# Performance work log

Hardware: AMD Instinct MI355X
Metric: run time of the kernel (lower is better)

Reference implementation:

```python
import jax, jax.numpy as jnp
import numpy as np

DIM = 1024
N_HEADS = 16
HEAD_DIM = DIM // N_HEADS
LN_EPS = 1e-5


def layer_norm(x, gamma, beta):
    mu = jnp.mean(x, axis=-1, keepdims=True)
    var = jnp.var(x, axis=-1, keepdims=True)
    return (x - mu) * jax.lax.rsqrt(var + LN_EPS) * gamma + beta


def setup_inputs() -> dict:
    key = jax.random.key(0)
    ks = jax.random.split(key, 12)
    B, Nq, Nc, D = 2, 2048, 2048, DIM
    s = 1.0 / np.sqrt(D)
    return {
        "query": jax.random.normal(ks[0], (B, Nq, D), jnp.float32),
        "context": jax.random.normal(ks[1], (B, Nc, D), jnp.float32),
        "Wq": jax.random.normal(ks[2], (D, D), jnp.float32) * s,
        "bq": jnp.zeros((D,), jnp.float32),
        "Wk": jax.random.normal(ks[3], (D, D), jnp.float32) * s,
        "bk": jnp.zeros((D,), jnp.float32),
        "Wv": jax.random.normal(ks[4], (D, D), jnp.float32) * s,
        "bv": jnp.zeros((D,), jnp.float32),
        "Wo": jax.random.normal(ks[5], (D, D), jnp.float32) * s,
        "bo": jnp.zeros((D,), jnp.float32),
        "gq": jnp.ones((D,), jnp.float32),
        "betaq": jnp.zeros((D,), jnp.float32),
        "gkv": jnp.ones((D,), jnp.float32),
        "betakv": jnp.zeros((D,), jnp.float32),
    }


def reference(query, context, Wq, bq, Wk, bk, Wv, bv, Wo, bo, gq, betaq, gkv, betakv):
    B, Nq, D = query.shape
    Nc = context.shape[1]
    residual = query
    q = layer_norm(query, gq, betaq)
    c = layer_norm(context, gkv, betakv)
    # projections; (B,N,D) -> (B,H,N,hd)
    Q = (q @ Wq + bq).reshape(B, Nq, N_HEADS, HEAD_DIM).transpose(0, 2, 1, 3)
    K = (c @ Wk + bk).reshape(B, Nc, N_HEADS, HEAD_DIM).transpose(0, 2, 1, 3)
    V = (c @ Wv + bv).reshape(B, Nc, N_HEADS, HEAD_DIM).transpose(0, 2, 1, 3)
    scores = jnp.einsum("bhqd,bhkd->bhqk", Q, K) / np.sqrt(HEAD_DIM).astype(np.float32)
    attn = jax.nn.softmax(scores, axis=-1)
    out = jnp.einsum("bhqk,bhkd->bhqd", attn, V)
    out = out.transpose(0, 2, 1, 3).reshape(B, Nq, D)
    return residual + out @ Wo + bo
```

## Files before the change

kernel.cpp:

```cpp
#include <hip/hip_runtime.h>
#include <hip/hip_bf16.h>

typedef unsigned short u16;
typedef unsigned long long u64;
typedef __bf16 bf16x8 __attribute__((ext_vector_type(8)));
typedef float f32x4 __attribute__((ext_vector_type(4)));
typedef float f32x16 __attribute__((ext_vector_type(16)));
typedef unsigned u32x4 __attribute__((ext_vector_type(4)));

#define DIM 1024
#define NH 16
#define HD 64
#define QSCALE 0.180336880972788f

__device__ __forceinline__ u16 f2bf(float f) {
  union { float f; unsigned u; } v; v.f = f;
  unsigned r = v.u + 0x7fffu + ((v.u >> 16) & 1u);
  return (u16)(r >> 16);
}

__device__ __forceinline__ unsigned pk2(float a, float b) {
  union { __hip_bfloat162 h; unsigned u; } cv;
  cv.h = __float22bfloat162_rn(make_float2(a, b));
  return cv.u;
}

__device__ __forceinline__ float bf2f(unsigned s) {
  union { unsigned u; float f; } v; v.u = s << 16; return v.f;
}

__device__ __forceinline__ float fexp2(float x) {
#if __has_builtin(__builtin_amdgcn_exp2f)
  return __builtin_amdgcn_exp2f(x);
#else
  return exp2f(x);
#endif
}

__device__ __forceinline__ void gld16(const u16* gp, u16* lp) {
  __builtin_amdgcn_global_load_lds(
      (const __attribute__((address_space(1))) unsigned int*)(const void*)gp,
      (__attribute__((address_space(3))) unsigned int*)(void*)lp, 16, 0, 0);
}

__device__ __forceinline__ void pl32swap(unsigned& a, unsigned& b) {
  asm volatile("v_permlane32_swap_b32 %0, %1" : "+v"(a), "+v"(b));
}

__global__ __launch_bounds__(256) void prep_kernel(
    const float* __restrict__ q, const float* __restrict__ c,
    const float* __restrict__ gq, const float* __restrict__ bq,
    const float* __restrict__ gkv, const float* __restrict__ bkv,
    u16* __restrict__ qn, u16* __restrict__ cn,
    const float* W0, const float* W1, const float* W2, const float* W3,
    u16* O0, u16* O1, u16* O2, u16* O3) {
  __shared__ float red[2][4];
  __shared__ float t[32][33];
  int bid = blockIdx.x, tid = threadIdx.x;
  if (bid < 8192) {
    const float* x  = bid < 4096 ? q : c;
    const float* g  = bid < 4096 ? gq : gkv;
    const float* be = bid < 4096 ? bq : bkv;
    u16* out = bid < 4096 ? qn : cn;
    int row = bid & 4095;
    float4 v = ((const float4*)(x + (size_t)row * DIM))[tid];
    float s1 = v.x + v.y + v.z + v.w;
    float s2 = v.x * v.x + v.y * v.y + v.z * v.z + v.w * v.w;
#pragma unroll
    for (int o = 32; o >= 1; o >>= 1) { s1 += __shfl_xor(s1, o, 64); s2 += __shfl_xor(s2, o, 64); }
    int wv = tid >> 6;
    if ((tid & 63) == 0) { red[0][wv] = s1; red[1][wv] = s2; }
    __syncthreads();
    s1 = red[0][0] + red[0][1] + red[0][2] + red[0][3];
    s2 = red[1][0] + red[1][1] + red[1][2] + red[1][3];
    float mu = s1 * (1.f / DIM);
    float var = s2 * (1.f / DIM) - mu * mu;
    float rs = rsqrtf(var + 1e-5f);
    float4 gv = ((const float4*)g)[tid];
    float4 bv = ((const float4*)be)[tid];
    uint2 o2;
    o2.x = pk2((v.x - mu) * rs * gv.x + bv.x, (v.y - mu) * rs * gv.y + bv.y);
    o2.y = pk2((v.z - mu) * rs * gv.z + bv.z, (v.w - mu) * rs * gv.w + bv.w);
    ((uint2*)(out + (size_t)row * DIM))[tid] = o2;
  } else {
    int wid = bid - 8192;
    int z = wid >> 10;
    const float* W = z == 0 ? W0 : z == 1 ? W1 : z == 2 ? W2 : W3;
    u16* O        = z == 0 ? O0 : z == 1 ? O1 : z == 2 ? O2 : O3;
    int xy = wid & 1023;
    int bx = (xy & 31) * 32, by = (xy >> 5) * 32;
    int tx = tid & 31, ty = tid >> 5;
#pragma unroll
    for (int i = 0; i < 4; ++i) t[ty + i * 8][tx] = W[(size_t)(by + ty + i * 8) * DIM + bx + tx];
    __syncthreads();
#pragma unroll
    for (int i = 0; i < 4; ++i) O[(size_t)(bx + ty + i * 8) * DIM + by + tx] = f2bf(t[tx][ty + i * 8]);
  }
}

__global__ __launch_bounds__(256) void gemm_qkv(
    const u16* __restrict__ qn, const u16* __restrict__ cn,
    const u16* __restrict__ Wqt, const u16* __restrict__ Wkt, const u16* __restrict__ Wvt,
    const float* __restrict__ bq, const float* __restrict__ bk, const float* __restrict__ bv,
    u16* __restrict__ Qb, u16* __restrict__ Kb, u16* __restrict__ Vtb) {
  __shared__ __align__(16) u16 sm[(128 + 64 + 64) * 64];
  u16* As  = sm;
  u16* B0s = sm + 128 * 64;
  u16* B1s = sm + 192 * 64;
  int tid = threadIdx.x, wave = tid >> 6, lane = tid & 63;
  int lr = lane & 15, quad = lane >> 4;
  int m0 = blockIdx.x * 128, n0 = blockIdx.y * 64;
  int wm = (wave >> 1) * 64, wn = (wave & 1) * 32;

  if (blockIdx.z == 0) {
    f32x4 acck[4][2] = {}, accv[4][2] = {};
    for (int kt = 0; kt < DIM; kt += 64) {
#pragma unroll
      for (int r = 0; r < 4; ++r) {
        int slot = tid + r * 256;
        int row = slot >> 3;
        int c = (slot & 7) ^ (row & 7);
        gld16(cn + (size_t)(m0 + row) * DIM + kt + c * 8, &As[slot * 8]);
      }
      {
        int slot = tid;
        int row = slot >> 3;
        int c = (slot & 7) ^ (row & 7);
        gld16(Wkt + (size_t)(n0 + row) * DIM + kt + c * 8, &B0s[slot * 8]);
        gld16(Wvt + (size_t)(n0 + row) * DIM + kt + c * 8, &B1s[slot * 8]);
        slot = tid + 256; row = slot >> 3; c = (slot & 7) ^ (row & 7);
        gld16(Wkt + (size_t)(n0 + row) * DIM + kt + c * 8, &B0s[slot * 8]);
        gld16(Wvt + (size_t)(n0 + row) * DIM + kt + c * 8, &B1s[slot * 8]);
      }
      __syncthreads();
#pragma unroll
      for (int kc = 0; kc < 2; ++kc) {
        int pc = ((kc * 4 + quad) ^ (lr & 7)) * 8;
        bf16x8 af[4], b0f[2], b1f[2];
#pragma unroll
        for (int i = 0; i < 4; ++i) af[i] = *(const bf16x8*)&As[(wm + i * 16 + lr) * 64 + pc];
#pragma unroll
        for (int j = 0; j < 2; ++j) {
          b0f[j] = *(const bf16x8*)&B0s[(wn + j * 16 + lr) * 64 + pc];
          b1f[j] = *(const bf16x8*)&B1s[(wn + j * 16 + lr) * 64 + pc];
        }
#pragma unroll
        for (int mi = 0; mi < 4; ++mi)
#pragma unroll
          for (int ni = 0; ni < 2; ++ni) {
            acck[mi][ni] = __builtin_amdgcn_mfma_f32_16x16x32_bf16(af[mi], b0f[ni], acck[mi][ni], 0, 0, 0);
            accv[mi][ni] = __builtin_amdgcn_mfma_f32_16x16x32_bf16(b1f[ni], af[mi], accv[mi][ni], 0, 0, 0);
          }
      }
      __syncthreads();
    }
#pragma unroll
    for (int mi = 0; mi < 4; ++mi)
#pragma unroll
      for (int ni = 0; ni < 2; ++ni) {
        int col = n0 + wn + ni * 16 + lr;
        float bb_ = bk[col];
        int row0 = m0 + wm + mi * 16 + quad * 4;
#pragma unroll
        for (int r = 0; r < 4; ++r)
          Kb[(size_t)(row0 + r) * DIM + col] = f2bf(acck[mi][ni][r] + bb_);
      }
#pragma unroll
    for (int mi = 0; mi < 4; ++mi) {
      int m = m0 + wm + mi * 16 + lr;
      int bb = m >> 11, tt = m & 2047;
      u16* outb = Vtb + (((size_t)bb << 10)) * 2048 + tt;
#pragma unroll
      for (int ni = 0; ni < 2; ++ni) {
        int nbase = n0 + wn + ni * 16 + quad * 4;
#pragma unroll
        for (int r = 0; r < 4; ++r)
          outb[(size_t)(nbase + r) * 2048] = f2bf(accv[mi][ni][r] + bv[nbase + r]);
      }
    }
  } else {
    f32x4 acc[4][2] = {};
    for (int kt = 0; kt < DIM; kt += 64) {
#pragma unroll
      for (int r = 0; r < 4; ++r) {
        int slot = tid + r * 256;
        int row = slot >> 3;
        int c = (slot & 7) ^ (row & 7);
        gld16(qn + (size_t)(m0 + row) * DIM + kt + c * 8, &As[slot * 8]);
      }
#pragma unroll
      for (int r = 0; r < 2; ++r) {
        int slot = tid + r * 256;
        int row = slot >> 3;
        int c = (slot & 7) ^ (row & 7);
        gld16(Wqt + (size_t)(n0 + row) * DIM + kt + c * 8, &B0s[slot * 8]);
      }
      __syncthreads();
#pragma unroll
      for (int kc = 0; kc < 2; ++kc) {
        int pc = ((kc * 4 + quad) ^ (lr & 7)) * 8;
        bf16x8 af[4], b0f[2];
#pragma unroll
        for (int i = 0; i < 4; ++i) af[i] = *(const bf16x8*)&As[(wm + i * 16 + lr) * 64 + pc];
#pragma unroll
        for (int j = 0; j < 2; ++j) b0f[j] = *(const bf16x8*)&B0s[(wn + j * 16 + lr) * 64 + pc];
#pragma unroll
        for (int mi = 0; mi < 4; ++mi)
#pragma unroll
          for (int ni = 0; ni < 2; ++ni)
            acc[mi][ni] = __builtin_amdgcn_mfma_f32_16x16x32_bf16(af[mi], b0f[ni], acc[mi][ni], 0, 0, 0);
      }
      __syncthreads();
    }
#pragma unroll
    for (int mi = 0; mi < 4; ++mi)
#pragma unroll
      for (int ni = 0; ni < 2; ++ni) {
        int col = n0 + wn + ni * 16 + lr;
        float bb_ = bq[col];
        int row0 = m0 + wm + mi * 16 + quad * 4;
#pragma unroll
        for (int r = 0; r < 4; ++r)
          Qb[(size_t)(row0 + r) * DIM + col] = f2bf((acc[mi][ni][r] + bb_) * QSCALE);
      }
  }
}

__global__ __launch_bounds__(256) void gemm_o(const u16* __restrict__ A,
    const u16* __restrict__ Bt, const float* __restrict__ bias,
    float* __restrict__ out, const float* __restrict__ resid) {
  __shared__ __align__(16) u16 sm[(128 + 64) * 64];
  u16* As = sm;
  u16* Bs = sm + 128 * 64;
  int tid = threadIdx.x, wave = tid >> 6, lane = tid & 63;
  int lr = lane & 15, quad = lane >> 4;
  int m0 = blockIdx.x * 128, n0 = blockIdx.y * 64;
  int wm = (wave >> 1) * 64, wn = (wave & 1) * 32;
  f32x4 acc[4][2] = {};
  for (int kt = 0; kt < DIM; kt += 64) {
#pragma unroll
    for (int r = 0; r < 4; ++r) {
      int slot = tid + r * 256;
      int row = slot >> 3;
      int c = (slot & 7) ^ (row & 7);
      gld16(A + (size_t)(m0 + row) * DIM + kt + c * 8, &As[slot * 8]);
    }
#pragma unroll
    for (int r = 0; r < 2; ++r) {
      int slot = tid + r * 256;
      int row = slot >> 3;
      int c = (slot & 7) ^ (row & 7);
      gld16(Bt + (size_t)(n0 + row) * DIM + kt + c * 8, &Bs[slot * 8]);
    }
    __syncthreads();
#pragma unroll
    for (int kc = 0; kc < 2; ++kc) {
      int pc = ((kc * 4 + quad) ^ (lr & 7)) * 8;
      bf16x8 af[4], bfr[2];
#pragma unroll
      for (int i = 0; i < 4; ++i) af[i] = *(const bf16x8*)&As[(wm + i * 16 + lr) * 64 + pc];
#pragma unroll
      for (int j = 0; j < 2; ++j) bfr[j] = *(const bf16x8*)&Bs[(wn + j * 16 + lr) * 64 + pc];
#pragma unroll
      for (int mi = 0; mi < 4; ++mi)
#pragma unroll
        for (int ni = 0; ni < 2; ++ni)
          acc[mi][ni] = __builtin_amdgcn_mfma_f32_16x16x32_bf16(af[mi], bfr[ni], acc[mi][ni], 0, 0, 0);
    }
    __syncthreads();
  }
#pragma unroll
  for (int mi = 0; mi < 4; ++mi)
#pragma unroll
    for (int ni = 0; ni < 2; ++ni) {
      int col = n0 + wn + ni * 16 + lr;
      float bv = bias[col];
      int row0 = m0 + wm + mi * 16 + quad * 4;
#pragma unroll
      for (int r = 0; r < 4; ++r) {
        int row = row0 + r;
        out[(size_t)row * DIM + col] = acc[mi][ni][r] + bv + resid[(size_t)row * DIM + col];
      }
    }
}

__global__ __launch_bounds__(256, 4) void flash_kernel(const u16* __restrict__ Q,
    const u16* __restrict__ Kg, const u16* __restrict__ Vt,
    u16* __restrict__ O0, u16* __restrict__ O1,
    float* __restrict__ L0, float* __restrict__ L1) {
  __shared__ __align__(16) u16 lds[16384];
  int tid = threadIdx.x, wave = tid >> 6, lane = tid & 63;
  int ln = lane & 31, hi = lane >> 5;
  int bh = blockIdx.x, b = bh >> 4, h = bh & 15;
  int q0 = blockIdx.y * 128;
  int split = blockIdx.z;
  u16* Op = split ? O1 : O0;
  float* Lp = split ? L1 : L0;
  int t0 = split * 1024;

  const u16* kbase = Kg + (size_t)(b * 2048 + t0) * DIM + h * HD;
  const u16* vbase = Vt + (size_t)(b * 1024 + h * HD) * 2048 + t0;

  size_t qrow = (size_t)(b * 2048 + q0 + wave * 32 + ln);
  bf16x8 qf[4];
#pragma unroll
  for (int ds = 0; ds < 4; ++ds)
    qf[ds] = *(const bf16x8*)&Q[qrow * DIM + h * HD + ds * 16 + hi * 8];

  int slot0 = tid, slot1 = tid + 256;
  int r0 = slot0 >> 3, c0 = (slot0 & 7) ^ (r0 & 7);
  int r1 = slot1 >> 3, c1 = (slot1 & 7) ^ (r1 & 7);
  const u16* kp0 = kbase + (size_t)r0 * DIM + c0 * 8;
  const u16* kp1 = kbase + (size_t)r1 * DIM + c1 * 8;
  const u16* vp0 = vbase + (size_t)r0 * 2048 + c0 * 8;
  const u16* vp1 = vbase + (size_t)r1 * 2048 + c1 * 8;

  gld16(kp0, &lds[slot0 * 8]);
  gld16(kp1, &lds[slot1 * 8]);
  gld16(vp0, &lds[8192 + slot0 * 8]);
  gld16(vp1, &lds[8192 + slot1 * 8]);
  __syncthreads();

  float plsum = 0.f;
  f32x16 oacc[2] = {};

  for (int j = 0; j < 16; ++j) {
    int par = j & 1;
    const u16* kcb = &lds[par * 4096];
    const u16* vcb = &lds[8192 + par * 4096];
    if (j < 15) {
      int np = par ^ 1;
      kp0 += 64 * DIM; kp1 += 64 * DIM; vp0 += 64; vp1 += 64;
      gld16(kp0, &lds[np * 4096 + slot0 * 8]);
      gld16(kp1, &lds[np * 4096 + slot1 * 8]);
      gld16(vp0, &lds[8192 + np * 4096 + slot0 * 8]);
      gld16(vp1, &lds[8192 + np * 4096 + slot1 * 8]);
    }

    f32x16 sf[2] = {};
    __builtin_amdgcn_s_setprio(1);
#pragma unroll
    for (int kt2 = 0; kt2 < 2; ++kt2) {
      int rs = (kt2 * 32 + ln) * 64;
      int rx = (kt2 * 32 + ln) & 7;
#pragma unroll
      for (int ds = 0; ds < 4; ++ds) {
        bf16x8 kf = *(const bf16x8*)&kcb[rs + (((ds * 2 + hi) ^ rx) * 8)];
        sf[kt2] = __builtin_amdgcn_mfma_f32_32x32x16_bf16(kf, qf[ds], sf[kt2], 0, 0, 0);
      }
    }
    __builtin_amdgcn_s_setprio(0);

    bf16x8 pb[4];
#pragma unroll
    for (int kt2 = 0; kt2 < 2; ++kt2)
#pragma unroll
      for (int ks = 0; ks < 2; ++ks) {
        float e0 = fexp2(sf[kt2][ks * 8 + 0]), e1 = fexp2(sf[kt2][ks * 8 + 1]);
        float e2 = fexp2(sf[kt2][ks * 8 + 2]), e3 = fexp2(sf[kt2][ks * 8 + 3]);
        float e4 = fexp2(sf[kt2][ks * 8 + 4]), e5 = fexp2(sf[kt2][ks * 8 + 5]);
        float e6 = fexp2(sf[kt2][ks * 8 + 6]), e7 = fexp2(sf[kt2][ks * 8 + 7]);
        plsum += ((e0 + e1) + (e2 + e3)) + ((e4 + e5) + (e6 + e7));
        unsigned w0 = pk2(e0, e1), w1 = pk2(e2, e3);
        unsigned w2 = pk2(e4, e5), w3 = pk2(e6, e7);
        pl32swap(w0, w2);
        pl32swap(w1, w3);
        u32x4 t; t.x = w0; t.y = w1; t.z = w2; t.w = w3;
        pb[kt2 * 2 + ks] = __builtin_bit_cast(bf16x8, t);
      }

    __builtin_amdgcn_s_setprio(1);
#pragma unroll
    for (int dt = 0; dt < 2; ++dt) {
      int rs = (dt * 32 + ln) * 64;
      int rx = (dt * 32 + ln) & 7;
#pragma unroll
      for (int kk = 0; kk < 4; ++kk) {
        bf16x8 vf = *(const bf16x8*)&vcb[rs + (((kk * 2 + hi) ^ rx) * 8)];
        oacc[dt] = __builtin_amdgcn_mfma_f32_32x32x16_bf16(vf, pb[kk], oacc[dt], 0, 0, 0);
      }
    }
    __builtin_amdgcn_s_setprio(0);
    __syncthreads();
  }

  float l = plsum + __shfl_xor(plsum, 32, 64);
  if (hi == 0) Lp[qrow * 16 + h] = l;
#pragma unroll
  for (int dt = 0; dt < 2; ++dt)
#pragma unroll
    for (int g = 0; g < 4; ++g) {
      uint2 pk;
      pk.x = pk2(oacc[dt][g * 4 + 0], oacc[dt][g * 4 + 1]);
      pk.y = pk2(oacc[dt][g * 4 + 2], oacc[dt][g * 4 + 3]);
      *(uint2*)&Op[qrow * DIM + h * HD + dt * 32 + g * 8 + hi * 4] = pk;
    }
}

__global__ __launch_bounds__(256) void combine_kernel(const u16* __restrict__ O0,
    const u16* __restrict__ O1, const float* __restrict__ L0, const float* __restrict__ L1,
    u16* __restrict__ AO) {
  int row = blockIdx.x, tid = threadIdx.x;
  int h = tid >> 4;
  float rl = 1.f / (L0[row * 16 + h] + L1[row * 16 + h]);
  uint2 a = ((const uint2*)(O0 + (size_t)row * DIM))[tid];
  uint2 b = ((const uint2*)(O1 + (size_t)row * DIM))[tid];
  float v0 = (bf2f(a.x & 0xffff) + bf2f(b.x & 0xffff)) * rl;
  float v1 = (bf2f(a.x >> 16)    + bf2f(b.x >> 16))    * rl;
  float v2 = (bf2f(a.y & 0xffff) + bf2f(b.y & 0xffff)) * rl;
  float v3 = (bf2f(a.y >> 16)    + bf2f(b.y >> 16))    * rl;
  uint2 o;
  o.x = pk2(v0, v1);
  o.y = pk2(v2, v3);
  ((uint2*)(AO + (size_t)row * DIM))[tid] = o;
}

extern "C" void kernel_launch(void* const* d_in, const int* in_sizes, int n_in,
                              void* d_out, int out_size, void* d_ws, size_t ws_size,
                              hipStream_t stream) {
  const float* query   = (const float*)d_in[0];
  const float* context = (const float*)d_in[1];
  const float* Wq = (const float*)d_in[2];
  const float* bq = (const float*)d_in[3];
  const float* Wk = (const float*)d_in[4];
  const float* bk = (const float*)d_in[5];
  const float* Wv = (const float*)d_in[6];
  const float* bv = (const float*)d_in[7];
  const float* Wo = (const float*)d_in[8];
  const float* bo = (const float*)d_in[9];
  const float* gq    = (const float*)d_in[10];
  const float* betaq = (const float*)d_in[11];
  const float* gkv   = (const float*)d_in[12];
  const float* betakv= (const float*)d_in[13];
  (void)in_sizes; (void)n_in; (void)out_size; (void)ws_size;

  char* ws = (char*)d_ws;
  const size_t MB = (size_t)1 << 20;
  u16* qn  = (u16*)(ws + 0 * MB);
  u16* cn  = (u16*)(ws + 8 * MB);
  u16* Wqt = (u16*)(ws + 16 * MB);
  u16* Wkt = (u16*)(ws + 18 * MB);
  u16* Wvt = (u16*)(ws + 20 * MB);
  u16* Wot = (u16*)(ws + 22 * MB);
  u16* Qb  = (u16*)(ws + 24 * MB);
  u16* Kb  = (u16*)(ws + 32 * MB);
  u16* Vtb = (u16*)(ws + 40 * MB);
  u16* AOb = (u16*)(ws + 48 * MB);
  u16* Op0 = qn;
  u16* Op1 = cn;
  float* L0 = (float*)(ws + 16 * MB);
  float* L1 = (float*)(ws + 16 * MB + 256 * 1024);

  prep_kernel<<<12288, 256, 0, stream>>>(query, context, gq, betaq, gkv, betakv,
                                         qn, cn, Wq, Wk, Wv, Wo, Wqt, Wkt, Wvt, Wot);

  gemm_qkv<<<dim3(32, 16, 2), 256, 0, stream>>>(qn, cn, Wqt, Wkt, Wvt,
                                                bq, bk, bv, Qb, Kb, Vtb);

  flash_kernel<<<dim3(32, 16, 2), 256, 0, stream>>>(Qb, Kb, Vtb, Op0, Op1, L0, L1);

  combine_kernel<<<4096, 256, 0, stream>>>(Op0, Op1, L0, L1, AOb);

  gemm_o<<<dim3(32, 16), 256, 0, stream>>>(AOb, Wot, bo, (float*)d_out, query);
}
```

Measured before the change: 215.2 us.

## Use 128x128 GEMM tiles and split QKV into three uniform z-slices

The QKV projection kernel drops the fused K+V block that shared one context tile across two weight matrices. It now uses a single 128x128 tile path with blockIdx.z selecting K, V (computed transposed) or Q, so every block does the same amount of work. The output projection GEMM also moves from 128x64 to 128x128 tiles, and both kernels declare three blocks per CU. Larger tiles give more MFMA work per LDS load and fewer blocks, at the cost of more accumulator registers, lower occupancy, and losing the shared A-tile reuse between K and V.

```diff
diff --git a/kernel.cpp b/kernel.cpp
--- a/kernel.cpp
+++ b/kernel.cpp
@@ -98,145 +98,23 @@
   }
 }
 
-__global__ __launch_bounds__(256) void gemm_qkv(
+__global__ __launch_bounds__(256, 3) void gemm_qkv(
     const u16* __restrict__ qn, const u16* __restrict__ cn,
     const u16* __restrict__ Wqt, const u16* __restrict__ Wkt, const u16* __restrict__ Wvt,
     const float* __restrict__ bq, const float* __restrict__ bk, const float* __restrict__ bv,
     u16* __restrict__ Qb, u16* __restrict__ Kb, u16* __restrict__ Vtb) {
-  __shared__ __align__(16) u16 sm[(128 + 64 + 64) * 64];
-  u16* As  = sm;
-  u16* B0s = sm + 128 * 64;
-  u16* B1s = sm + 192 * 64;
-  int tid = threadIdx.x, wave = tid >> 6, lane = tid & 63;
-  int lr = lane & 15, quad = lane >> 4;
-  int m0 = blockIdx.x * 128, n0 = blockIdx.y * 64;
-  int wm = (wave >> 1) * 64, wn = (wave & 1) * 32;
-
-  if (blockIdx.z == 0) {
-    f32x4 acck[4][2] = {}, accv[4][2] = {};
-    for (int kt = 0; kt < DIM; kt += 64) {
-#pragma unroll
-      for (int r = 0; r < 4; ++r) {
-        int slot = tid + r * 256;
-        int row = slot >> 3;
-        int c = (slot & 7) ^ (row & 7);
-        gld16(cn + (size_t)(m0 + row) * DIM + kt + c * 8, &As[slot * 8]);
-      }
-      {
-        int slot = tid;
-        int row = slot >> 3;
-        int c = (slot & 7) ^ (row & 7);
-        gld16(Wkt + (size_t)(n0 + row) * DIM + kt + c * 8, &B0s[slot * 8]);
-        gld16(Wvt + (size_t)(n0 + row) * DIM + kt + c * 8, &B1s[slot * 8]);
-        slot = tid + 256; row = slot >> 3; c = (slot & 7) ^ (row & 7);
-        gld16(Wkt + (size_t)(n0 + row) * DIM + kt + c * 8, &B0s[slot * 8]);
-        gld16(Wvt + (size_t)(n0 + row) * DIM + kt + c * 8, &B1s[slot * 8]);
-      }
-      __syncthreads();
-#pragma unroll
-      for (int kc = 0; kc < 2; ++kc) {
-        int pc = ((kc * 4 + quad) ^ (lr & 7)) * 8;
-        bf16x8 af[4], b0f[2], b1f[2];
-#pragma unroll
-        for (int i = 0; i < 4; ++i) af[i] = *(const bf16x8*)&As[(wm + i * 16 + lr) * 64 + pc];
-#pragma unroll
-        for (int j = 0; j < 2; ++j) {
-          b0f[j] = *(const bf16x8*)&B0s[(wn + j * 16 + lr) * 64 + pc];
-          b1f[j] = *(const bf16x8*)&B1s[(wn + j * 16 + lr) * 64 + pc];
-        }
-#pragma unroll
-        for (int mi = 0; mi < 4; ++mi)
-#pragma unroll
-          for (int ni = 0; ni < 2; ++ni) {
-            acck[mi][ni] = __builtin_amdgcn_mfma_f32_16x16x32_bf16(af[mi], b0f[ni], acck[mi][ni], 0, 0, 0);
-            accv[mi][ni] = __builtin_amdgcn_mfma_f32_16x16x32_bf16(b1f[ni], af[mi], accv[mi][ni], 0, 0, 0);
-          }
-      }
-      __syncthreads();
-    }
-#pragma unroll
-    for (int mi = 0; mi < 4; ++mi)
-#pragma unroll
-      for (int ni = 0; ni < 2; ++ni) {
-        int col = n0 + wn + ni * 16 + lr;
-        float bb_ = bk[col];
-        int row0 = m0 + wm + mi * 16 + quad * 4;
-#pragma unroll
-        for (int r = 0; r < 4; ++r)
-          Kb[(size_t)(row0 + r) * DIM + col] = f2bf(acck[mi][ni][r] + bb_);
-      }
-#pragma unroll
-    for (int mi = 0; mi < 4; ++mi) {
-      int m = m0 + wm + mi * 16 + lr;
-      int bb = m >> 11, tt = m & 2047;
-      u16* outb = Vtb + (((size_t)bb << 10)) * 2048 + tt;
-#pragma unroll
-      for (int ni = 0; ni < 2; ++ni) {
-        int nbase = n0 + wn + ni * 16 + quad * 4;
-#pragma unroll
-        for (int r = 0; r < 4; ++r)
-          outb[(size_t)(nbase + r) * 2048] = f2bf(accv[mi][ni][r] + bv[nbase + r]);
-      }
-    }
-  } else {
-    f32x4 acc[4][2] = {};
-    for (int kt = 0; kt < DIM; kt += 64) {
-#pragma unroll
-      for (int r = 0; r < 4; ++r) {
-        int slot = tid + r * 256;
-        int row = slot >> 3;
-        int c = (slot & 7) ^ (row & 7);
-        gld16(qn + (size_t)(m0 + row) * DIM + kt + c * 8, &As[slot * 8]);
-      }
-#pragma unroll
-      for (int r = 0; r < 2; ++r) {
-        int slot = tid + r * 256;
-        int row = slot >> 3;
-        int c = (slot & 7) ^ (row & 7);
-        gld16(Wqt + (size_t)(n0 + row) * DIM + kt + c * 8, &B0s[slot * 8]);
-      }
-      __syncthreads();
-#pragma unroll
-      for (int kc = 0; kc < 2; ++kc) {
-        int pc = ((kc * 4 + quad) ^ (lr & 7)) * 8;
-        bf16x8 af[4], b0f[2];
-#pragma unroll
-        for (int i = 0; i < 4; ++i) af[i] = *(const bf16x8*)&As[(wm + i * 16 + lr) * 64 + pc];
-#pragma unroll
-        for (int j = 0; j < 2; ++j) b0f[j] = *(const bf16x8*)&B0s[(wn + j * 16 + lr) * 64 + pc];
-#pragma unroll
-        for (int mi = 0; mi < 4; ++mi)
-#pragma unroll
-          for (int ni = 0; ni < 2; ++ni)
-            acc[mi][ni] = __builtin_amdgcn_mfma_f32_16x16x32_bf16(af[mi], b0f[ni], acc[mi][ni], 0, 0, 0);
-      }
-      __syncthreads();
-    }
-#pragma unroll
-    for (int mi = 0; mi < 4; ++mi)
-#pragma unroll
-      for (int ni = 0; ni < 2; ++ni) {
-        int col = n0 + wn + ni * 16 + lr;
-        float bb_ = bq[col];
-        int row0 = m0 + wm + mi * 16 + quad * 4;
-#pragma unroll
-        for (int r = 0; r < 4; ++r)
-          Qb[(size_t)(row0 + r) * DIM + col] = f2bf((acc[mi][ni][r] + bb_) * QSCALE);
-      }
-  }
-}
-
-__global__ __launch_bounds__(256) void gemm_o(const u16* __restrict__ A,
-    const u16* __restrict__ Bt, const float* __restrict__ bias,
-    float* __restrict__ out, const float* __restrict__ resid) {
-  __shared__ __align__(16) u16 sm[(128 + 64) * 64];
+  __shared__ __align__(16) u16 sm[(128 + 128) * 64];
   u16* As = sm;
   u16* Bs = sm + 128 * 64;
   int tid = threadIdx.x, wave = tid >> 6, lane = tid & 63;
   int lr = lane & 15, quad = lane >> 4;
-  int m0 = blockIdx.x * 128, n0 = blockIdx.y * 64;
-  int wm = (wave >> 1) * 64, wn = (wave & 1) * 32;
-  f32x4 acc[4][2] = {};
+  int z = blockIdx.z;
+  const u16* A = (z == 2) ? qn : cn;
+  const u16* W = (z == 0) ? Wkt : (z == 1) ? Wvt : Wqt;
+  int m0 = blockIdx.x * 128, n0 = blockIdx.y * 128;
+  int wm = (wave >> 1) * 64, wn = (wave & 1) * 64;
+
+  f32x4 acc[4][4] = {};
   for (int kt = 0; kt < DIM; kt += 64) {
 #pragma unroll
     for (int r = 0; r < 4; ++r) {
@@ -244,27 +122,99 @@
       int row = slot >> 3;
       int c = (slot & 7) ^ (row & 7);
       gld16(A + (size_t)(m0 + row) * DIM + kt + c * 8, &As[slot * 8]);
-    }
-#pragma unroll
-    for (int r = 0; r < 2; ++r) {
+      gld16(W + (size_t)(n0 + row) * DIM + kt + c * 8, &Bs[slot * 8]);
+    }
+    __syncthreads();
+#pragma unroll
+    for (int kc = 0; kc < 2; ++kc) {
+      int pc = ((kc * 4 + quad) ^ (lr & 7)) * 8;
+      bf16x8 af[4], bf[4];
+#pragma unroll
+      for (int i = 0; i < 4; ++i) af[i] = *(const bf16x8*)&As[(wm + i * 16 + lr) * 64 + pc];
+#pragma unroll
+      for (int j = 0; j < 4; ++j) bf[j] = *(const bf16x8*)&Bs[(wn + j * 16 + lr) * 64 + pc];
+      if (z == 1) {
+#pragma unroll
+        for (int mi = 0; mi < 4; ++mi)
+#pragma unroll
+          for (int ni = 0; ni < 4; ++ni)
+            acc[mi][ni] = __builtin_amdgcn_mfma_f32_16x16x32_bf16(bf[ni], af[mi], acc[mi][ni], 0, 0, 0);
+      } else {
+#pragma unroll
+        for (int mi = 0; mi < 4; ++mi)
+#pragma unroll
+          for (int ni = 0; ni < 4; ++ni)
+            acc[mi][ni] = __builtin_amdgcn_mfma_f32_16x16x32_bf16(af[mi], bf[ni], acc[mi][ni], 0, 0, 0);
+      }
+    }
+    __syncthreads();
+  }
+
+  if (z == 1) {
+#pragma unroll
+    for (int mi = 0; mi < 4; ++mi) {
+      int m = m0 + wm + mi * 16 + lr;
+      int bb = m >> 11, tt = m & 2047;
+      u16* outb = Vtb + (((size_t)bb << 10)) * 2048 + tt;
+#pragma unroll
+      for (int ni = 0; ni < 4; ++ni) {
+        int nbase = n0 + wn + ni * 16 + quad * 4;
+#pragma unroll
+        for (int r = 0; r < 4; ++r)
+          outb[(size_t)(nbase + r) * 2048] = f2bf(acc[mi][ni][r] + bv[nbase + r]);
+      }
+    }
+  } else {
+    const float* bias = (z == 0) ? bk : bq;
+    u16* out = (z == 0) ? Kb : Qb;
+    float scale = (z == 0) ? 1.f : QSCALE;
+#pragma unroll
+    for (int mi = 0; mi < 4; ++mi)
+#pragma unroll
+      for (int ni = 0; ni < 4; ++ni) {
+        int col = n0 + wn + ni * 16 + lr;
+        float bb_ = bias[col];
+        int row0 = m0 + wm + mi * 16 + quad * 4;
+#pragma unroll
+        for (int r = 0; r < 4; ++r)
+          out[(size_t)(row0 + r) * DIM + col] = f2bf((acc[mi][ni][r] + bb_) * scale);
+      }
+  }
+}
+
+__global__ __launch_bounds__(256, 3) void gemm_o(const u16* __restrict__ A,
+    const u16* __restrict__ Bt, const float* __restrict__ bias,
+    float* __restrict__ out, const float* __restrict__ resid) {
+  __shared__ __align__(16) u16 sm[(128 + 128) * 64];
+  u16* As = sm;
+  u16* Bs = sm + 128 * 64;
+  int tid = threadIdx.x, wave = tid >> 6, lane = tid & 63;
+  int lr = lane & 15, quad = lane >> 4;
+  int m0 = blockIdx.x * 128, n0 = blockIdx.y * 128;
+  int wm = (wave >> 1) * 64, wn = (wave & 1) * 64;
+  f32x4 acc[4][4] = {};
+  for (int kt = 0; kt < DIM; kt += 64) {
+#pragma unroll
+    for (int r = 0; r < 4; ++r) {
       int slot = tid + r * 256;
       int row = slot >> 3;
       int c = (slot & 7) ^ (row & 7);
+      gld16(A + (size_t)(m0 + row) * DIM + kt + c * 8, &As[slot * 8]);
       gld16(Bt + (size_t)(n0 + row) * DIM + kt + c * 8, &Bs[slot * 8]);
     }
     __syncthreads();
 #pragma unroll
     for (int kc = 0; kc < 2; ++kc) {
       int pc = ((kc * 4 + quad) ^ (lr & 7)) * 8;
-      bf16x8 af[4], bfr[2];
+      bf16x8 af[4], bfr[4];
 #pragma unroll
       for (int i = 0; i < 4; ++i) af[i] = *(const bf16x8*)&As[(wm + i * 16 + lr) * 64 + pc];
 #pragma unroll
-      for (int j = 0; j < 2; ++j) bfr[j] = *(const bf16x8*)&Bs[(wn + j * 16 + lr) * 64 + pc];
+      for (int j = 0; j < 4; ++j) bfr[j] = *(const bf16x8*)&Bs[(wn + j * 16 + lr) * 64 + pc];
 #pragma unroll
       for (int mi = 0; mi < 4; ++mi)
 #pragma unroll
-        for (int ni = 0; ni < 2; ++ni)
+        for (int ni = 0; ni < 4; ++ni)
           acc[mi][ni] = __builtin_amdgcn_mfma_f32_16x16x32_bf16(af[mi], bfr[ni], acc[mi][ni], 0, 0, 0);
     }
     __syncthreads();
@@ -272,7 +222,7 @@
 #pragma unroll
   for (int mi = 0; mi < 4; ++mi)
 #pragma unroll
-    for (int ni = 0; ni < 2; ++ni) {
+    for (int ni = 0; ni < 4; ++ni) {
       int col = n0 + wn + ni * 16 + lr;
       float bv = bias[col];
       int row0 = m0 + wm + mi * 16 + quad * 4;
@@ -454,12 +404,12 @@
   prep_kernel<<<12288, 256, 0, stream>>>(query, context, gq, betaq, gkv, betakv,
                                          qn, cn, Wq, Wk, Wv, Wo, Wqt, Wkt, Wvt, Wot);
 
-  gemm_qkv<<<dim3(32, 16, 2), 256, 0, stream>>>(qn, cn, Wqt, Wkt, Wvt,
-                                                bq, bk, bv, Qb, Kb, Vtb);
+  gemm_qkv<<<dim3(32, 8, 3), 256, 0, stream>>>(qn, cn, Wqt, Wkt, Wvt,
+                                               bq, bk, bv, Qb, Kb, Vtb);
 
   flash_kernel<<<dim3(32, 16, 2), 256, 0, stream>>>(Qb, Kb, Vtb, Op0, Op1, L0, L1);
 
   combine_kernel<<<4096, 256, 0, stream>>>(Op0, Op1, L0, L1, AOb);
 
-  gemm_o<<<dim3(32, 16), 256, 0, stream>>>(AOb, Wot, bo, (float*)d_out, query);
-}
+  gemm_o<<<dim3(32, 8), 256, 0, stream>>>(AOb, Wot, bo, (float*)d_out, query);
+}
```

Measured after the change: 264.0 us. 22.7% more time.

## Double-buffer LDS in QKV and output GEMMs; issue flash prefetch after QK MFMAs

Applied to the files above, without the earlier changes.

The QKV and output-projection GEMMs move from single-buffered LDS tiles to two buffers. Each iteration prefetches the next K-tile with direct global-to-LDS loads while computing on the current tile, then waits on vmcnt plus a barrier. In the flash kernel, the next K/V tile prefetch is now issued after the QK^T MFMAs instead of before them. This doubles GEMM LDS use, which may lower occupancy, and changes how prefetch latency overlaps with compute in attention.

```diff
diff --git a/kernel.cpp b/kernel.cpp
--- a/kernel.cpp
+++ b/kernel.cpp
@@ -45,6 +45,11 @@
 
 __device__ __forceinline__ void pl32swap(unsigned& a, unsigned& b) {
   asm volatile("v_permlane32_swap_b32 %0, %1" : "+v"(a), "+v"(b));
+}
+
+__device__ __forceinline__ void drain_vm_barrier() {
+  asm volatile("s_waitcnt vmcnt(0)" ::: "memory");
+  __builtin_amdgcn_s_barrier();
 }
 
 __global__ __launch_bounds__(256) void prep_kernel(
@@ -98,23 +103,23 @@
   }
 }
 
+#define QKV_BUF 16384
 __global__ __launch_bounds__(256) void gemm_qkv(
     const u16* __restrict__ qn, const u16* __restrict__ cn,
     const u16* __restrict__ Wqt, const u16* __restrict__ Wkt, const u16* __restrict__ Wvt,
     const float* __restrict__ bq, const float* __restrict__ bk, const float* __restrict__ bv,
     u16* __restrict__ Qb, u16* __restrict__ Kb, u16* __restrict__ Vtb) {
-  __shared__ __align__(16) u16 sm[(128 + 64 + 64) * 64];
-  u16* As  = sm;
-  u16* B0s = sm + 128 * 64;
-  u16* B1s = sm + 192 * 64;
+  __shared__ __align__(16) u16 sm[2 * QKV_BUF];
   int tid = threadIdx.x, wave = tid >> 6, lane = tid & 63;
   int lr = lane & 15, quad = lane >> 4;
   int m0 = blockIdx.x * 128, n0 = blockIdx.y * 64;
   int wm = (wave >> 1) * 64, wn = (wave & 1) * 32;
 
   if (blockIdx.z == 0) {
-    f32x4 acck[4][2] = {}, accv[4][2] = {};
-    for (int kt = 0; kt < DIM; kt += 64) {
+    auto stage = [&](int buf, int kt) {
+      u16* As  = sm + buf * QKV_BUF;
+      u16* B0s = As + 128 * 64;
+      u16* B1s = As + 192 * 64;
 #pragma unroll
       for (int r = 0; r < 4; ++r) {
         int slot = tid + r * 256;
@@ -122,17 +127,25 @@
         int c = (slot & 7) ^ (row & 7);
         gld16(cn + (size_t)(m0 + row) * DIM + kt + c * 8, &As[slot * 8]);
       }
-      {
-        int slot = tid;
+#pragma unroll
+      for (int r = 0; r < 2; ++r) {
+        int slot = tid + r * 256;
         int row = slot >> 3;
         int c = (slot & 7) ^ (row & 7);
         gld16(Wkt + (size_t)(n0 + row) * DIM + kt + c * 8, &B0s[slot * 8]);
         gld16(Wvt + (size_t)(n0 + row) * DIM + kt + c * 8, &B1s[slot * 8]);
-        slot = tid + 256; row = slot >> 3; c = (slot & 7) ^ (row & 7);
-        gld16(Wkt + (size_t)(n0 + row) * DIM + kt + c * 8, &B0s[slot * 8]);
-        gld16(Wvt + (size_t)(n0 + row) * DIM + kt + c * 8, &B1s[slot * 8]);
-      }
-      __syncthreads();
+      }
+    };
+
+    f32x4 acck[4][2] = {}, accv[4][2] = {};
+    stage(0, 0);
+    drain_vm_barrier();
+    int cur = 0;
+    for (int kt = 0; kt < DIM; kt += 64) {
+      if (kt + 64 < DIM) stage(cur ^ 1, kt + 64);
+      const u16* As  = sm + cur * QKV_BUF;
+      const u16* B0s = As + 128 * 64;
+      const u16* B1s = As + 192 * 64;
 #pragma unroll
       for (int kc = 0; kc < 2; ++kc) {
         int pc = ((kc * 4 + quad) ^ (lr & 7)) * 8;
@@ -152,7 +165,8 @@
             accv[mi][ni] = __builtin_amdgcn_mfma_f32_16x16x32_bf16(b1f[ni], af[mi], accv[mi][ni], 0, 0, 0);
           }
       }
-      __syncthreads();
+      drain_vm_barrier();
+      cur ^= 1;
     }
 #pragma unroll
     for (int mi = 0; mi < 4; ++mi)
@@ -179,8 +193,9 @@
       }
     }
   } else {
-    f32x4 acc[4][2] = {};
-    for (int kt = 0; kt < DIM; kt += 64) {
+    auto stage = [&](int buf, int kt) {
+      u16* As  = sm + buf * QKV_BUF;
+      u16* B0s = As + 128 * 64;
 #pragma unroll
       for (int r = 0; r < 4; ++r) {
         int slot = tid + r * 256;
@@ -195,7 +210,16 @@
         int c = (slot & 7) ^ (row & 7);
         gld16(Wqt + (size_t)(n0 + row) * DIM + kt + c * 8, &B0s[slot * 8]);
       }
-      __syncthreads();
+    };
+
+    f32x4 acc[4][2] = {};
+    stage(0, 0);
+    drain_vm_barrier();
+    int cur = 0;
+    for (int kt = 0; kt < DIM; kt += 64) {
+      if (kt + 64 < DIM) stage(cur ^ 1, kt + 64);
+      const u16* As  = sm + cur * QKV_BUF;
+      const u16* B0s = As + 128 * 64;
 #pragma unroll
       for (int kc = 0; kc < 2; ++kc) {
         int pc = ((kc * 4 + quad) ^ (lr & 7)) * 8;
@@ -210,7 +234,8 @@
           for (int ni = 0; ni < 2; ++ni)
             acc[mi][ni] = __builtin_amdgcn_mfma_f32_16x16x32_bf16(af[mi], b0f[ni], acc[mi][ni], 0, 0, 0);
       }
-      __syncthreads();
+      drain_vm_barrier();
+      cur ^= 1;
     }
 #pragma unroll
     for (int mi = 0; mi < 4; ++mi)
@@ -226,18 +251,19 @@
   }
 }
 
+#define O_BUF 12288
 __global__ __launch_bounds__(256) void gemm_o(const u16* __restrict__ A,
     const u16* __restrict__ Bt, const float* __restrict__ bias,
     float* __restrict__ out, const float* __restrict__ resid) {
-  __shared__ __align__(16) u16 sm[(128 + 64) * 64];
-  u16* As = sm;
-  u16* Bs = sm + 128 * 64;
+  __shared__ __align__(16) u16 sm[2 * O_BUF];
   int tid = threadIdx.x, wave = tid >> 6, lane = tid & 63;
   int lr = lane & 15, quad = lane >> 4;
   int m0 = blockIdx.x * 128, n0 = blockIdx.y * 64;
   int wm = (wave >> 1) * 64, wn = (wave & 1) * 32;
-  f32x4 acc[4][2] = {};
-  for (int kt = 0; kt < DIM; kt += 64) {
+
+  auto stage = [&](int buf, int kt) {
+    u16* As = sm + buf * O_BUF;
+    u16* Bs = As + 128 * 64;
 #pragma unroll
     for (int r = 0; r < 4; ++r) {
       int slot = tid + r * 256;
@@ -252,7 +278,16 @@
       int c = (slot & 7) ^ (row & 7);
       gld16(Bt + (size_t)(n0 + row) * DIM + kt + c * 8, &Bs[slot * 8]);
     }
-    __syncthreads();
+  };
+
+  f32x4 acc[4][2] = {};
+  stage(0, 0);
+  drain_vm_barrier();
+  int cur = 0;
+  for (int kt = 0; kt < DIM; kt += 64) {
+    if (kt + 64 < DIM) stage(cur ^ 1, kt + 64);
+    const u16* As = sm + cur * O_BUF;
+    const u16* Bs = As + 128 * 64;
 #pragma unroll
     for (int kc = 0; kc < 2; ++kc) {
       int pc = ((kc * 4 + quad) ^ (lr & 7)) * 8;
@@ -267,7 +302,8 @@
         for (int ni = 0; ni < 2; ++ni)
           acc[mi][ni] = __builtin_amdgcn_mfma_f32_16x16x32_bf16(af[mi], bfr[ni], acc[mi][ni], 0, 0, 0);
     }
-    __syncthreads();
+    drain_vm_barrier();
+    cur ^= 1;
   }
 #pragma unroll
   for (int mi = 0; mi < 4; ++mi)
@@ -328,6 +364,21 @@
     int par = j & 1;
     const u16* kcb = &lds[par * 4096];
     const u16* vcb = &lds[8192 + par * 4096];
+
+    f32x16 sf[2] = {};
+    __builtin_amdgcn_s_setprio(1);
+#pragma unroll
+    for (int kt2 = 0; kt2 < 2; ++kt2) {
+      int rs = (kt2 * 32 + ln) * 64;
+      int rx = (kt2 * 32 + ln) & 7;
+#pragma unroll
+      for (int ds = 0; ds < 4; ++ds) {
+        bf16x8 kf = *(const bf16x8*)&kcb[rs + (((ds * 2 + hi) ^ rx) * 8)];
+        sf[kt2] = __builtin_amdgcn_mfma_f32_32x32x16_bf16(kf, qf[ds], sf[kt2], 0, 0, 0);
+      }
+    }
+    __builtin_amdgcn_s_setprio(0);
+
     if (j < 15) {
       int np = par ^ 1;
       kp0 += 64 * DIM; kp1 += 64 * DIM; vp0 += 64; vp1 += 64;
@@ -336,20 +387,6 @@
       gld16(vp0, &lds[8192 + np * 4096 + slot0 * 8]);
       gld16(vp1, &lds[8192 + np * 4096 + slot1 * 8]);
     }
-
-    f32x16 sf[2] = {};
-    __builtin_amdgcn_s_setprio(1);
-#pragma unroll
-    for (int kt2 = 0; kt2 < 2; ++kt2) {
-      int rs = (kt2 * 32 + ln) * 64;
-      int rx = (kt2 * 32 + ln) & 7;
-#pragma unroll
-      for (int ds = 0; ds < 4; ++ds) {
-        bf16x8 kf = *(const bf16x8*)&kcb[rs + (((ds * 2 + hi) ^ rx) * 8)];
-        sf[kt2] = __builtin_amdgcn_mfma_f32_32x32x16_bf16(kf, qf[ds], sf[kt2], 0, 0, 0);
-      }
-    }
-    __builtin_amdgcn_s_setprio(0);
 
     bf16x8 pb[4];
 #pragma unroll
```

After: 204.6 us. 1.05x faster.
